# Kernel optimization log

Hardware: AMD Instinct MI355X
Metric: run time of the kernel (lower is better)

## Reference

```python
import jax, jax.numpy as jnp
import numpy as np

D_MODEL = 512
NUM_HEADS = 8
HEAD_DIM = D_MODEL // NUM_HEADS
ATTN_WINDOW = 256


def setup_inputs() -> dict:
    key = jax.random.key(0)
    ks = jax.random.split(key, 5)
    B, S = 2, 4096
    x = jax.random.normal(ks[0], (B, S, D_MODEL), dtype=jnp.float32)
    s = 1.0 / np.sqrt(D_MODEL)
    qkv_w = jax.random.uniform(ks[1], (3 * D_MODEL, D_MODEL), minval=-s, maxval=s, dtype=jnp.float32)
    qkv_b = jax.random.uniform(ks[2], (3 * D_MODEL,), minval=-s, maxval=s, dtype=jnp.float32)
    out_w = jax.random.uniform(ks[3], (D_MODEL, D_MODEL), minval=-s, maxval=s, dtype=jnp.float32)
    out_b = jax.random.uniform(ks[4], (D_MODEL,), minval=-s, maxval=s, dtype=jnp.float32)
    return {"x": x, "qkv_w": qkv_w, "qkv_b": qkv_b, "out_w": out_w, "out_b": out_b}


def reference(x, qkv_w, qkv_b, out_w, out_b):
    B, S, D = x.shape
    scale = HEAD_DIM ** (-0.5)
    qkv = x @ qkv_w.T + qkv_b                       # [B,S,3D]
    qkv = qkv.reshape(B, S, 3, NUM_HEADS, HEAD_DIM)
    q, k, v = qkv[:, :, 0], qkv[:, :, 1], qkv[:, :, 2]
    scores = jnp.einsum('bthd,bshd->bhts', q, k) * scale  # [B,H,S,S]
    i = jnp.arange(S)[:, None]
    j = jnp.arange(S)[None, :]
    # causal AND within sliding window of size ATTN_WINDOW
    mask = (j <= i) & (j >= i - ATTN_WINDOW)        # [S,S] bool
    scores = jnp.where(mask, scores, -jnp.inf)
    weights = jax.nn.softmax(scores, axis=-1)
    out = jnp.einsum('bhts,bshd->bthd', weights, v).reshape(B, S, D)
    return out @ out_w.T + out_b
```

## Files before the change

### kernel.cpp

```cpp
#include <hip/hip_runtime.h>

#define S_LEN 4096
#define BATCH 2
#define DM 512
#define NH 8
#define DH 64
#define WINDOW 256

typedef __bf16 bf16x8 __attribute__((ext_vector_type(8)));
typedef float f32x4 __attribute__((ext_vector_type(4)));
typedef unsigned short u16x8 __attribute__((ext_vector_type(8)));

typedef const __attribute__((address_space(1))) unsigned int* gas_ptr;
typedef __attribute__((address_space(3))) unsigned int* las_ptr;

__device__ __forceinline__ unsigned short f2bf(float f) {
  unsigned int u = __float_as_uint(f);
  u += 0x7fffu + ((u >> 16) & 1u);
  return (unsigned short)(u >> 16);
}

__global__ __launch_bounds__(256) void convert_bf16(const float* __restrict__ src,
                                                    unsigned short* __restrict__ dst, int n4) {
  int i = blockIdx.x * blockDim.x + threadIdx.x;
  const int stride = gridDim.x * blockDim.x;
  for (; i < n4; i += stride) {
    const float4 v = ((const float4*)src)[i];
    ushort4 o;
    o.x = f2bf(v.x); o.y = f2bf(v.y); o.z = f2bf(v.z); o.w = f2bf(v.w);
    ((ushort4*)dst)[i] = o;
  }
}

__device__ __forceinline__ void gemm_core(const unsigned short* __restrict__ A,
                                          const unsigned short* __restrict__ Bm,
                                          int m0, int n0,
                                          unsigned short* sA, unsigned short* sB,
                                          f32x4 acc[4][4]) {
  const int t = threadIdx.x;
  const int wave = t >> 6, lane = t & 63;
  const int wr = wave >> 1, wc = wave & 1;
  const int quad = lane >> 4, l16 = lane & 15;

  for (int k0 = 0; k0 < 512; k0 += 32) {
#pragma unroll
    for (int p = 0; p < 2; ++p) {
      const int ci = wave * 128 + p * 64 + lane;
      const int row = ci >> 2, cg = ci & 3;
      const unsigned short* ga = A + (size_t)(m0 + row) * 512 + k0 + cg * 8;
      __builtin_amdgcn_global_load_lds((gas_ptr)(const void*)ga,
                                       (las_ptr)(void*)(sA + wave * 1024 + p * 512), 16, 0, 0);
      const unsigned short* gb = Bm + (size_t)(n0 + row) * 512 + k0 + cg * 8;
      __builtin_amdgcn_global_load_lds((gas_ptr)(const void*)gb,
                                       (las_ptr)(void*)(sB + wave * 1024 + p * 512), 16, 0, 0);
    }
    __syncthreads();
    bf16x8 af[4], bff[4];
#pragma unroll
    for (int i = 0; i < 4; ++i)
      af[i] = *(const bf16x8*)&sA[(wr * 64 + i * 16 + l16) * 32 + quad * 8];
#pragma unroll
    for (int j = 0; j < 4; ++j)
      bff[j] = *(const bf16x8*)&sB[(wc * 64 + j * 16 + l16) * 32 + quad * 8];
#pragma unroll
    for (int i = 0; i < 4; ++i)
#pragma unroll
      for (int j = 0; j < 4; ++j)
        acc[i][j] = __builtin_amdgcn_mfma_f32_16x16x32_bf16(af[i], bff[j], acc[i][j], 0, 0, 0);
    __syncthreads();
  }
}

__global__ __launch_bounds__(256) void gemm_qkv(const unsigned short* __restrict__ xb,
                                                const unsigned short* __restrict__ wb,
                                                const float* __restrict__ bias,
                                                unsigned short* __restrict__ Qb,
                                                unsigned short* __restrict__ Kb,
                                                unsigned short* __restrict__ Vt) {
  __shared__ __align__(16) unsigned short sA[128 * 32];
  __shared__ __align__(16) unsigned short sB[128 * 32];
  f32x4 acc[4][4] = {};
  const int m0 = blockIdx.y * 128, n0 = blockIdx.x * 128;
  gemm_core(xb, wb, m0, n0, sA, sB, acc);

  const int t = threadIdx.x;
  const int wave = t >> 6, lane = t & 63;
  const int wr = wave >> 1, wc = wave & 1;
  const int quad = lane >> 4, l16 = lane & 15;
#pragma unroll
  for (int j = 0; j < 4; ++j) {
    const int n = n0 + wc * 64 + j * 16 + l16;
    const float bv = bias[n];
#pragma unroll
    for (int i = 0; i < 4; ++i) {
      const int mr = m0 + wr * 64 + i * 16 + quad * 4;
      if (n < DM) {
#pragma unroll
        for (int r = 0; r < 4; ++r)
          Qb[(size_t)(mr + r) * DM + n] = f2bf(acc[i][j][r] + bv);
      } else if (n < 2 * DM) {
#pragma unroll
        for (int r = 0; r < 4; ++r)
          Kb[(size_t)(mr + r) * DM + (n - DM)] = f2bf(acc[i][j][r] + bv);
      } else {
        const int d = n & 63, h = (n - 2 * DM) >> 6;
#pragma unroll
        for (int r = 0; r < 4; ++r) {
          const int m = mr + r;
          const int b = m >> 12, s = m & (S_LEN - 1);
          Vt[((size_t)((b * NH + h) * DH + d)) * S_LEN + s] = f2bf(acc[i][j][r] + bv);
        }
      }
    }
  }
}

__global__ __launch_bounds__(256) void gemm_out(const unsigned short* __restrict__ Ab,
                                                const unsigned short* __restrict__ wb,
                                                const float* __restrict__ bias,
                                                float* __restrict__ C) {
  __shared__ __align__(16) unsigned short sA[128 * 32];
  __shared__ __align__(16) unsigned short sB[128 * 32];
  f32x4 acc[4][4] = {};
  const int m0 = blockIdx.y * 128, n0 = blockIdx.x * 128;
  gemm_core(Ab, wb, m0, n0, sA, sB, acc);

  const int t = threadIdx.x;
  const int wave = t >> 6, lane = t & 63;
  const int wr = wave >> 1, wc = wave & 1;
  const int quad = lane >> 4, l16 = lane & 15;
#pragma unroll
  for (int j = 0; j < 4; ++j) {
    const int n = n0 + wc * 64 + j * 16 + l16;
    const float bv = bias[n];
#pragma unroll
    for (int i = 0; i < 4; ++i) {
      const int mr = m0 + wr * 64 + i * 16 + quad * 4;
#pragma unroll
      for (int r = 0; r < 4; ++r)
        C[(size_t)(mr + r) * DM + n] = acc[i][j][r] + bv;
    }
  }
}

__global__ __launch_bounds__(256) void attn_mfma(const unsigned short* __restrict__ Qb,
                                                 const unsigned short* __restrict__ Kb,
                                                 const unsigned short* __restrict__ Vt,
                                                 unsigned short* __restrict__ AO) {
  __shared__ __align__(16) unsigned short Qs[64 * 72];
  __shared__ __align__(16) unsigned short Ks[64 * 72];
  __shared__ __align__(16) unsigned short Vs[64 * 72];
  __shared__ __align__(16) unsigned short Ps[64 * 72];
  const int t = threadIdx.x;
  const int wave = t >> 6, lane = t & 63;
  const int quad = lane >> 4, l16 = lane & 15;
  const int q0 = blockIdx.x * 64, h = blockIdx.y, b = blockIdx.z;

#pragma unroll
  for (int s = 0; s < 2; ++s) {
    const int f = t + 256 * s;
    const int row = f >> 3, cg = f & 7;
    *(u16x8*)&Qs[row * 72 + cg * 8] =
        *(const u16x8*)(Qb + (size_t)(b * S_LEN + q0 + row) * DM + h * DH + cg * 8);
  }

  float m_[4], l_[4];
  f32x4 O[4] = {};
#pragma unroll
  for (int r = 0; r < 4; ++r) { m_[r] = -1e30f; l_[r] = 0.f; }

  for (int c = 0; c < 5; ++c) {
    const int c0 = q0 - WINDOW + c * 64;
    if (c0 < 0) continue;
    __syncthreads();
#pragma unroll
    for (int s = 0; s < 2; ++s) {
      const int f = t + 256 * s;
      const int row = f >> 3, cg = f & 7;
      *(u16x8*)&Ks[row * 72 + cg * 8] =
          *(const u16x8*)(Kb + (size_t)(b * S_LEN + c0 + row) * DM + h * DH + cg * 8);
      *(u16x8*)&Vs[row * 72 + cg * 8] =
          *(const u16x8*)(Vt + ((size_t)((b * NH + h) * DH + row)) * S_LEN + c0 + cg * 8);
    }
    __syncthreads();

    bf16x8 aq0 = *(const bf16x8*)&Qs[(wave * 16 + l16) * 72 + quad * 8];
    bf16x8 aq1 = *(const bf16x8*)&Qs[(wave * 16 + l16) * 72 + 32 + quad * 8];
    f32x4 sc[4];
#pragma unroll
    for (int nt = 0; nt < 4; ++nt) {
      bf16x8 bk0 = *(const bf16x8*)&Ks[(nt * 16 + l16) * 72 + quad * 8];
      bf16x8 bk1 = *(const bf16x8*)&Ks[(nt * 16 + l16) * 72 + 32 + quad * 8];
      f32x4 z = {};
      z = __builtin_amdgcn_mfma_f32_16x16x32_bf16(aq0, bk0, z, 0, 0, 0);
      sc[nt] = __builtin_amdgcn_mfma_f32_16x16x32_bf16(aq1, bk1, z, 0, 0, 0);
    }

    float rmax[4];
#pragma unroll
    for (int r = 0; r < 4; ++r) rmax[r] = -1e30f;
#pragma unroll
    for (int nt = 0; nt < 4; ++nt) {
      const int j = c0 + nt * 16 + l16;
#pragma unroll
      for (int r = 0; r < 4; ++r) {
        const int i = q0 + wave * 16 + quad * 4 + r;
        const bool ok = (j <= i) && (j >= i - WINDOW);
        const float v = ok ? sc[nt][r] * 0.125f : -1e30f;
        sc[nt][r] = v;
        rmax[r] = fmaxf(rmax[r], v);
      }
    }
#pragma unroll
    for (int off = 1; off <= 8; off <<= 1)
#pragma unroll
      for (int r = 0; r < 4; ++r) rmax[r] = fmaxf(rmax[r], __shfl_xor(rmax[r], off));

    float alpha[4], csum[4];
#pragma unroll
    for (int r = 0; r < 4; ++r) {
      const float mn = fmaxf(m_[r], rmax[r]);
      alpha[r] = __expf(m_[r] - mn);
      m_[r] = mn;
      float su = 0.f;
#pragma unroll
      for (int nt = 0; nt < 4; ++nt) {
        const float p = __expf(sc[nt][r] - mn);
        sc[nt][r] = p;
        su += p;
      }
      csum[r] = su;
    }
#pragma unroll
    for (int off = 1; off <= 8; off <<= 1)
#pragma unroll
      for (int r = 0; r < 4; ++r) csum[r] += __shfl_xor(csum[r], off);
#pragma unroll
    for (int r = 0; r < 4; ++r) l_[r] = l_[r] * alpha[r] + csum[r];

#pragma unroll
    for (int nt = 0; nt < 4; ++nt)
#pragma unroll
      for (int r = 0; r < 4; ++r)
        Ps[(wave * 16 + quad * 4 + r) * 72 + nt * 16 + l16] = f2bf(sc[nt][r]);

    bf16x8 ap0 = *(const bf16x8*)&Ps[(wave * 16 + l16) * 72 + quad * 8];
    bf16x8 ap1 = *(const bf16x8*)&Ps[(wave * 16 + l16) * 72 + 32 + quad * 8];
#pragma unroll
    for (int nt = 0; nt < 4; ++nt) {
#pragma unroll
      for (int r = 0; r < 4; ++r) O[nt][r] *= alpha[r];
      bf16x8 bv0 = *(const bf16x8*)&Vs[(nt * 16 + l16) * 72 + quad * 8];
      bf16x8 bv1 = *(const bf16x8*)&Vs[(nt * 16 + l16) * 72 + 32 + quad * 8];
      O[nt] = __builtin_amdgcn_mfma_f32_16x16x32_bf16(ap0, bv0, O[nt], 0, 0, 0);
      O[nt] = __builtin_amdgcn_mfma_f32_16x16x32_bf16(ap1, bv1, O[nt], 0, 0, 0);
    }
  }

#pragma unroll
  for (int r = 0; r < 4; ++r) l_[r] = 1.f / l_[r];
#pragma unroll
  for (int nt = 0; nt < 4; ++nt) {
    const int col = h * DH + nt * 16 + l16;
#pragma unroll
    for (int r = 0; r < 4; ++r) {
      const int m = b * S_LEN + q0 + wave * 16 + quad * 4 + r;
      AO[(size_t)m * DM + col] = f2bf(O[nt][r] * l_[r]);
    }
  }
}

extern "C" void kernel_launch(void* const* d_in, const int* in_sizes, int n_in,
                              void* d_out, int out_size, void* d_ws, size_t ws_size,
                              hipStream_t stream) {
  const float* x = (const float*)d_in[0];
  const float* qkv_w = (const float*)d_in[1];
  const float* qkv_b = (const float*)d_in[2];
  const float* out_w = (const float*)d_in[3];
  const float* out_b = (const float*)d_in[4];
  float* out = (float*)d_out;

  const int M = BATCH * S_LEN;
  unsigned short* ws = (unsigned short*)d_ws;
  unsigned short* xb   = ws;
  unsigned short* wqkv = xb + (size_t)M * DM;
  unsigned short* wout = wqkv + 3 * DM * DM;
  unsigned short* Qb   = wout + DM * DM;
  unsigned short* Kb   = Qb + (size_t)M * DM;
  unsigned short* Vt   = Kb + (size_t)M * DM;
  unsigned short* AO   = Vt + (size_t)M * DM;

  convert_bf16<<<1024, 256, 0, stream>>>(x, xb, M * DM / 4);
  convert_bf16<<<768, 256, 0, stream>>>(qkv_w, wqkv, 3 * DM * DM / 4);
  convert_bf16<<<256, 256, 0, stream>>>(out_w, wout, DM * DM / 4);

  gemm_qkv<<<dim3(3 * DM / 128, M / 128), 256, 0, stream>>>(xb, wqkv, qkv_b, Qb, Kb, Vt);

  attn_mfma<<<dim3(S_LEN / 64, NH, BATCH), 256, 0, stream>>>(Qb, Kb, Vt, AO);

  gemm_out<<<dim3(DM / 128, M / 128), 256, 0, stream>>>(AO, wout, out_b, out);
}
```

Before: 150.9 us.

## Prefetch K/V chunks into registers, fuse converts, simplify masking and use exp2

The attention kernel now loads the next K/V chunk into registers while the current one is computed, double-buffering through registers to hide global load latency. The chunk loop is fully unrolled, and the mask is applied only on the first and last chunks using local indices. The softmax scale is folded into log2e so exp2f replaces __expf. The three bf16 conversion launches are merged into one kernel to cut launch overhead, at the cost of extra registers for the prefetch buffers.

```diff
diff --git a/kernel.cpp b/kernel.cpp
--- a/kernel.cpp
+++ b/kernel.cpp
@@ -14,22 +14,31 @@
 typedef const __attribute__((address_space(1))) unsigned int* gas_ptr;
 typedef __attribute__((address_space(3))) unsigned int* las_ptr;
 
+#define SCALE_LOG2E 0.1803368801111204f
+
 __device__ __forceinline__ unsigned short f2bf(float f) {
   unsigned int u = __float_as_uint(f);
   u += 0x7fffu + ((u >> 16) & 1u);
   return (unsigned short)(u >> 16);
 }
 
-__global__ __launch_bounds__(256) void convert_bf16(const float* __restrict__ src,
-                                                    unsigned short* __restrict__ dst, int n4) {
-  int i = blockIdx.x * blockDim.x + threadIdx.x;
-  const int stride = gridDim.x * blockDim.x;
-  for (; i < n4; i += stride) {
-    const float4 v = ((const float4*)src)[i];
-    ushort4 o;
-    o.x = f2bf(v.x); o.y = f2bf(v.y); o.z = f2bf(v.z); o.w = f2bf(v.w);
-    ((ushort4*)dst)[i] = o;
-  }
+#define N4_X (8192 * 512 / 4)
+#define N4_QW (1536 * 512 / 4)
+#define N4_OW (512 * 512 / 4)
+__global__ __launch_bounds__(256) void convert_all(const float* __restrict__ x,
+                                                   const float* __restrict__ qw,
+                                                   const float* __restrict__ ow,
+                                                   unsigned short* __restrict__ dst) {
+  const int i = blockIdx.x * blockDim.x + threadIdx.x;
+  const float4* src;
+  int off;
+  if (i < N4_X) { src = (const float4*)x; off = 0; }
+  else if (i < N4_X + N4_QW) { src = (const float4*)qw; off = N4_X; }
+  else { src = (const float4*)ow; off = N4_X + N4_QW; }
+  const float4 v = src[i - off];
+  ushort4 o;
+  o.x = f2bf(v.x); o.y = f2bf(v.y); o.z = f2bf(v.z); o.w = f2bf(v.w);
+  ((ushort4*)dst)[i] = o;
 }
 
 __device__ __forceinline__ void gemm_core(const unsigned short* __restrict__ A,
@@ -156,6 +165,9 @@
   const int quad = lane >> 4, l16 = lane & 15;
   const int q0 = blockIdx.x * 64, h = blockIdx.y, b = blockIdx.z;
 
+  const unsigned short* Kbase = Kb + (size_t)b * S_LEN * DM + h * DH;
+  const unsigned short* Vbase = Vt + (size_t)((b * NH + h) * DH) * S_LEN;
+
 #pragma unroll
   for (int s = 0; s < 2; ++s) {
     const int f = t + 256 * s;
@@ -164,24 +176,41 @@
         *(const u16x8*)(Qb + (size_t)(b * S_LEN + q0 + row) * DM + h * DH + cg * 8);
   }
 
+  const int first = (q0 >= WINDOW) ? 0 : (4 - blockIdx.x);
+
+  u16x8 kbuf[2][2], vbuf[2][2];
+#define LOAD_CHUNK(c0, p)                                                      \
+  do {                                                                         \
+    _Pragma("unroll") for (int s = 0; s < 2; ++s) {                            \
+      const int f = t + 256 * s;                                               \
+      const int row = f >> 3, c8 = f & 7;                                      \
+      kbuf[p][s] = *(const u16x8*)(Kbase + (size_t)((c0) + row) * DM + c8 * 8);\
+      vbuf[p][s] = *(const u16x8*)(Vbase + (size_t)row * S_LEN + (c0) + c8 * 8);\
+    }                                                                          \
+  } while (0)
+
+#pragma unroll
+  for (int c = 0; c < 5; ++c)
+    if (c == first) LOAD_CHUNK(q0 - WINDOW + c * 64, c & 1);
+
   float m_[4], l_[4];
   f32x4 O[4] = {};
 #pragma unroll
   for (int r = 0; r < 4; ++r) { m_[r] = -1e30f; l_[r] = 0.f; }
 
+#pragma unroll
   for (int c = 0; c < 5; ++c) {
+    if (c < first) continue;
     const int c0 = q0 - WINDOW + c * 64;
-    if (c0 < 0) continue;
     __syncthreads();
 #pragma unroll
     for (int s = 0; s < 2; ++s) {
       const int f = t + 256 * s;
-      const int row = f >> 3, cg = f & 7;
-      *(u16x8*)&Ks[row * 72 + cg * 8] =
-          *(const u16x8*)(Kb + (size_t)(b * S_LEN + c0 + row) * DM + h * DH + cg * 8);
-      *(u16x8*)&Vs[row * 72 + cg * 8] =
-          *(const u16x8*)(Vt + ((size_t)((b * NH + h) * DH + row)) * S_LEN + c0 + cg * 8);
-    }
+      const int row = f >> 3, c8 = f & 7;
+      *(u16x8*)&Ks[row * 72 + c8 * 8] = kbuf[c & 1][s];
+      *(u16x8*)&Vs[row * 72 + c8 * 8] = vbuf[c & 1][s];
+    }
+    if (c < 4) LOAD_CHUNK(c0 + 64, (c + 1) & 1);
     __syncthreads();
 
     bf16x8 aq0 = *(const bf16x8*)&Qs[(wave * 16 + l16) * 72 + quad * 8];
@@ -201,12 +230,13 @@
     for (int r = 0; r < 4; ++r) rmax[r] = -1e30f;
 #pragma unroll
     for (int nt = 0; nt < 4; ++nt) {
-      const int j = c0 + nt * 16 + l16;
+      const int jj = nt * 16 + l16;
 #pragma unroll
       for (int r = 0; r < 4; ++r) {
-        const int i = q0 + wave * 16 + quad * 4 + r;
-        const bool ok = (j <= i) && (j >= i - WINDOW);
-        const float v = ok ? sc[nt][r] * 0.125f : -1e30f;
+        const int ii = wave * 16 + quad * 4 + r;
+        float v = sc[nt][r] * SCALE_LOG2E;
+        if (c == 0) v = (jj >= ii) ? v : -1e30f;
+        if (c == 4) v = (jj <= ii) ? v : -1e30f;
         sc[nt][r] = v;
         rmax[r] = fmaxf(rmax[r], v);
       }
@@ -220,12 +250,12 @@
 #pragma unroll
     for (int r = 0; r < 4; ++r) {
       const float mn = fmaxf(m_[r], rmax[r]);
-      alpha[r] = __expf(m_[r] - mn);
+      alpha[r] = exp2f(m_[r] - mn);
       m_[r] = mn;
       float su = 0.f;
 #pragma unroll
       for (int nt = 0; nt < 4; ++nt) {
-        const float p = __expf(sc[nt][r] - mn);
+        const float p = exp2f(sc[nt][r] - mn);
         sc[nt][r] = p;
         su += p;
       }
@@ -290,9 +320,7 @@
   unsigned short* Vt   = Kb + (size_t)M * DM;
   unsigned short* AO   = Vt + (size_t)M * DM;
 
-  convert_bf16<<<1024, 256, 0, stream>>>(x, xb, M * DM / 4);
-  convert_bf16<<<768, 256, 0, stream>>>(qkv_w, wqkv, 3 * DM * DM / 4);
-  convert_bf16<<<256, 256, 0, stream>>>(out_w, wout, DM * DM / 4);
+  convert_all<<<(N4_X + N4_QW + N4_OW) / 256, 256, 0, stream>>>(x, qkv_w, out_w, xb);
 
   gemm_qkv<<<dim3(3 * DM / 128, M / 128), 256, 0, stream>>>(xb, wqkv, qkv_b, Qb, Kb, Vt);
 
```

After: 149.7 us. No clear change (-0.8%).
